# Kernel tuning notes

Hardware: AMD Instinct MI355X
Metric: run time of the kernel (lower is better)

The kernel has to match this reference:

```python
import jax, jax.numpy as jnp
import numpy as np

N = 50000      # nodes
E = 800000     # edges (avg degree 16)
H = 128        # hidden_dim
ED = 8         # edge_dim
TD = 64        # time_dim
EIN = 2 * H + 1 + ED + TD  # 329, phi_e input dim


def _linear_params(key, fan_in, fan_out):
    kw, kb = jax.random.split(key)
    s = 1.0 / np.sqrt(fan_in)
    W = jax.random.uniform(kw, (fan_in, fan_out), minval=-s, maxval=s, dtype=jnp.float32)
    b = jax.random.uniform(kb, (fan_out,), minval=-s, maxval=s, dtype=jnp.float32)
    return W, b


def setup_inputs() -> dict:
    key = jax.random.key(0)
    ks = jax.random.split(key, 12)
    h = jax.random.normal(ks[0], (N, H), dtype=jnp.float32)
    x = jax.random.normal(ks[1], (N, 3), dtype=jnp.float32)
    edge_attr = jax.random.normal(ks[2], (E, ED), dtype=jnp.float32)
    t_emb = jax.random.normal(ks[3], (N, TD), dtype=jnp.float32)
    edge_index = jax.random.randint(ks[4], (2, E), 0, N, dtype=jnp.int32)
    We1_w, We1_b = _linear_params(ks[5], EIN, H)
    We2_w, We2_b = _linear_params(ks[6], H, H)
    Watt_w, Watt_b = _linear_params(ks[7], H, 1)
    Wx1_w, Wx1_b = _linear_params(ks[8], H, H)
    Wx2_w, Wx2_b = _linear_params(ks[9], H, 1)
    Wh1_w, Wh1_b = _linear_params(ks[10], 2 * H, H)
    Wh2_w, Wh2_b = _linear_params(ks[11], H, H)
    return dict(h=h, x=x, edge_attr=edge_attr, t_emb=t_emb,
                We1_w=We1_w, We1_b=We1_b, We2_w=We2_w, We2_b=We2_b,
                Watt_w=Watt_w, Watt_b=Watt_b,
                Wx1_w=Wx1_w, Wx1_b=Wx1_b, Wx2_w=Wx2_w, Wx2_b=Wx2_b,
                Wh1_w=Wh1_w, Wh1_b=Wh1_b, Wh2_w=Wh2_w, Wh2_b=Wh2_b,
                edge_index=edge_index)


def reference(h, x, edge_attr, t_emb,
              We1_w, We1_b, We2_w, We2_b,
              Watt_w, Watt_b,
              Wx1_w, Wx1_b, Wx2_w, Wx2_b,
              Wh1_w, Wh1_b, Wh2_w, Wh2_b,
              edge_index):
    src, dst = edge_index[0], edge_index[1]
    diff = x[src] - x[dst]                                   # (E, 3)
    dist_sq = jnp.sum(diff * diff, axis=-1, keepdims=True)   # (E, 1)
    # m_ij = phi_e(h_i || h_j || ||x_i - x_j||^2 || edge_attr || t_emb)
    msg_in = jnp.concatenate([h[src], h[dst], dist_sq, edge_attr, t_emb[src]], axis=-1)  # (E, EIN)
    m = jax.nn.silu(msg_in @ We1_w + We1_b) @ We2_w + We2_b  # (E, H)
    # attention gate
    att = jax.nn.sigmoid(m @ Watt_w + Watt_b)                # (E, 1)
    m = att * m
    # equivariant coordinate update
    coord_w = jnp.tanh(jax.nn.silu(m @ Wx1_w + Wx1_b) @ Wx2_w + Wx2_b)  # (E, 1)
    coord_shift = diff * coord_w                             # (E, 3)
    coord_agg = jax.ops.segment_sum(coord_shift, dst, num_segments=N)   # (N, 3)
    deg = jax.ops.segment_sum(jnp.ones((dst.shape[0], 1), dtype=x.dtype), dst, num_segments=N)
    x_out = x + coord_agg / (deg + 1.0)
    # invariant feature update with residual
    msg_agg = jax.ops.segment_sum(m, dst, num_segments=N)    # (N, H)
    h_in = jnp.concatenate([h, msg_agg], axis=-1)            # (N, 2H)
    h_out = h + (jax.nn.silu(h_in @ Wh1_w + Wh1_b) @ Wh2_w + Wh2_b)
    return (h_out, x_out)
```

## Files before the change

### kernel.cpp

```cpp
#include <hip/hip_runtime.h>
#include <hip/hip_fp16.h>

typedef unsigned short u16;
typedef unsigned int u32;
typedef __attribute__((ext_vector_type(8))) short short8;
typedef __attribute__((ext_vector_type(4))) float f32x4;

#define NN 50000
#define EE 800000

__device__ __forceinline__ float bf2f(u16 u){ union{u32 i; float f;} v; v.i=((u32)u)<<16; return v.f; }
__device__ __forceinline__ u16 f2bf(float f){ union{float f; u32 i;} v; v.f=f; u32 b=v.i; b += 0x7FFFu + ((b>>16)&1u); return (u16)(b>>16); }
__device__ __forceinline__ float sigmoidf_(float x){ return 1.0f/(1.0f+__expf(-x)); }

__device__ __forceinline__ void cvt8(uint4 q, float* f){
  f[0]=bf2f((u16)(q.x&0xFFFF)); f[1]=bf2f((u16)(q.x>>16));
  f[2]=bf2f((u16)(q.y&0xFFFF)); f[3]=bf2f((u16)(q.y>>16));
  f[4]=bf2f((u16)(q.z&0xFFFF)); f[5]=bf2f((u16)(q.z>>16));
  f[6]=bf2f((u16)(q.w&0xFFFF)); f[7]=bf2f((u16)(q.w>>16));
}
__device__ __forceinline__ uint4 pack8(const float* f){
  uint4 q;
  q.x=(u32)f2bf(f[0])|((u32)f2bf(f[1])<<16);
  q.y=(u32)f2bf(f[2])|((u32)f2bf(f[3])<<16);
  q.z=(u32)f2bf(f[4])|((u32)f2bf(f[5])<<16);
  q.w=(u32)f2bf(f[6])|((u32)f2bf(f[7])<<16);
  return q;
}

__device__ __forceinline__ float h2f(u16 u){ __half h; *reinterpret_cast<u16*>(&h)=u; return (float)h; }
__device__ __forceinline__ u32 f2h2pack(float lo, float hi){
  __half2 h2 = __floats2half2_rn(lo, hi);
  return *reinterpret_cast<u32*>(&h2);
}
__device__ __forceinline__ void atomic_pk_add_f16(u16* addr, u32 data){
  asm volatile("global_atomic_pk_add_f16 %0, %1, off" :: "v"(addr), "v"(data) : "memory");
}

template<int FP32> struct IO;
template<> struct IO<0> {
  static __device__ __forceinline__ float ld(const void* p, int i){ return bf2f(((const u16*)p)[i]); }
  static __device__ __forceinline__ void ld8(const void* p, int i, float* f){
    cvt8(*(const uint4*)((const u16*)p + i), f);
  }
  static __device__ __forceinline__ void st(void* p, int i, float v){ ((u16*)p)[i] = f2bf(v); }
};
template<> struct IO<1> {
  static __device__ __forceinline__ float ld(const void* p, int i){ return ((const float*)p)[i]; }
  static __device__ __forceinline__ void ld8(const void* p, int i, float* f){
    f32x4 a = *(const f32x4*)((const float*)p + i);
    f32x4 b = *(const f32x4*)((const float*)p + i + 4);
    f[0]=a[0]; f[1]=a[1]; f[2]=a[2]; f[3]=a[3];
    f[4]=b[0]; f[5]=b[1]; f[6]=b[2]; f[7]=b[3];
  }
  static __device__ __forceinline__ void st(void* p, int i, float v){ ((float*)p)[i] = v; }
};

__device__ __forceinline__ void atomic_add_bf16pair(u32* addr, float lo, float hi){
  u32 old = *addr, assumed;
  do {
    assumed = old;
    float flo = bf2f((u16)(assumed & 0xFFFFu)) + lo;
    float fhi = bf2f((u16)(assumed >> 16)) + hi;
    u32 newv = (u32)f2bf(flo) | ((u32)f2bf(fhi) << 16);
    if (newv == assumed) return;
    old = atomicCAS(addr, assumed, newv);
  } while (old != assumed);
}

__global__ void k_probe(const u16* __restrict__ hraw, int* __restrict__ flag){
  if (threadIdx.x==0 && blockIdx.x==0){
    float mx = 0.f; int zc = 0;
    for (int i = 0; i < 256; i += 2){
      u16 u = hraw[i];
      if (u == 0) zc++;
      float v = fabsf(bf2f(u));
      mx = fmaxf(mx, v);
    }
    flag[0] = (mx > 1e3f || zc > 32) ? 1 : 0;
  }
}

template<int FP32>
__global__ __launch_bounds__(256) void k_prep(
    const int* __restrict__ flag,
    const void* __restrict__ We1, const void* __restrict__ We2,
    const void* __restrict__ Wx1, const void* __restrict__ Wh1,
    const void* __restrict__ Wh2,
    u16* __restrict__ WprojT, u16* __restrict__ We2T, u16* __restrict__ Wx1T,
    u16* __restrict__ Wh1T, u16* __restrict__ Wh2T, u16* __restrict__ Wrk9T)
{
  if (flag[0] != FP32) return;
  int i = blockIdx.x*256 + threadIdx.x;
  if (i < 49152){
    int n = i/192, k = i%192; float v;
    if (n < 128) v = (k<128) ? IO<FP32>::ld(We1, k*128+n) : IO<FP32>::ld(We1, (265+k-128)*128+n);
    else         v = (k<128) ? IO<FP32>::ld(We1, (128+k)*128+(n-128)) : 0.f;
    WprojT[i] = f2bf(v);
  } else if (i < 65536){
    int j=i-49152; int n=j/128, k=j%128; We2T[j] = f2bf(IO<FP32>::ld(We2, k*128+n));
  } else if (i < 81920){
    int j=i-65536; int n=j/128, k=j%128; Wx1T[j] = f2bf(IO<FP32>::ld(Wx1, k*128+n));
  } else if (i < 114688){
    int j=i-81920; int n=j/256, k=j%256; Wh1T[j] = f2bf(IO<FP32>::ld(Wh1, k*128+n));
  } else if (i < 131072){
    int j=i-114688; int n=j/128, k=j%128; Wh2T[j] = f2bf(IO<FP32>::ld(Wh2, k*128+n));
  } else if (i < 135168){
    int j=i-131072; int n=j/32, k=j%32;
    float v = (k<=8) ? IO<FP32>::ld(We1, (256+k)*128+n) : 0.f;
    Wrk9T[j] = f2bf(v);
  }
}

template<int FP32, int WP2>
__global__ __launch_bounds__(256) void k_proj(
    const int* __restrict__ flag,
    const void* __restrict__ h, const void* __restrict__ temb,
    const u16* __restrict__ WprojT, const void* __restrict__ We1b,
    u16* __restrict__ P13, u16* __restrict__ P2)
{
  if (flag[0] != FP32) return;
  constexpr int NT = WP2 ? 16 : 8;
  __shared__ __align__(16) u16 s_a[64][200];
  int tid = threadIdx.x; int nbase = blockIdx.x*64;
  {
    u32* p = (u32*)&s_a[0][0];
    for (int i = tid; i < 6400; i += 256) p[i] = 0u;
  }
  __syncthreads();
  {
    int r = tid>>2, p = tid&3; int node = nbase + r;
    if (node < NN){
      #pragma unroll
      for (int c=0;c<6;c++){
        int col = p*48 + c*8;
        float f[8];
        if (col<128) IO<FP32>::ld8(h, node*128 + col, f);
        else         IO<FP32>::ld8(temb, node*64 + (col-128), f);
        *(uint4*)&s_a[r][col] = pack8(f);
      }
    }
  }
  __syncthreads();
  int lane=tid&63, wid=tid>>6, quad=lane>>4, l15=lane&15, mb=wid*16;
  f32x4 acc[NT];
  #pragma unroll
  for (int nt=0;nt<NT;nt++) acc[nt]=(f32x4){0.f,0.f,0.f,0.f};
  #pragma unroll
  for (int ks=0;ks<6;ks++){
    short8 af = *(const short8*)&s_a[mb+l15][ks*32+quad*8];
    #pragma unroll
    for (int nt=0;nt<NT;nt++){
      short8 bfr = *(const short8*)(WprojT + (nt*16+l15)*192 + ks*32+quad*8);
      acc[nt] = __builtin_amdgcn_mfma_f32_16x16x32_bf16(af, bfr, acc[nt], 0,0,0);
    }
  }
  #pragma unroll
  for (int r=0;r<4;r++){
    int node = nbase + mb + quad*4 + r;
    if (node < NN){
      #pragma unroll
      for (int nt=0;nt<NT;nt++){
        int colg = nt*16 + l15;
        float v = acc[nt][r];
        if (colg < 128) P13[node*128+colg] = f2bf(v + IO<FP32>::ld(We1b, colg));
        else if (WP2)   P2[node*128+(colg-128)] = f2bf(v);
      }
    }
  }
}

template<int FP32, int TIERA>
__global__ __launch_bounds__(256, 6) void k_edge(
    const int* __restrict__ flag,
    const void* __restrict__ x, const void* __restrict__ ea,
    const void* __restrict__ We1, const void* __restrict__ h,
    const void* __restrict__ We2b, const void* __restrict__ Watt, const void* __restrict__ Wattb,
    const void* __restrict__ Wx1b, const void* __restrict__ Wx2, const void* __restrict__ Wx2b,
    const int* __restrict__ eidx,
    const u16* __restrict__ P13, const u16* __restrict__ P2,
    const u16* __restrict__ WprojT, const u16* __restrict__ Wrk9T,
    const u16* __restrict__ We2T, const u16* __restrict__ Wx1T,
    u16* __restrict__ msgh, u16* __restrict__ msgb, float* __restrict__ cagg)
{
  if (flag[0] != FP32) return;
  __shared__ int s_dst[64];
  __shared__ float s_dif[64][3];
  __shared__ __align__(16) u16 s_hid[64][136];
  __shared__ __align__(16) u16 s_att[TIERA?64:1][40];
  __shared__ __align__(16) u16 s_m[TIERA?1:64][136];
  __shared__ __align__(16) u16 s_hd[TIERA?1:64][136];
  int tid = threadIdx.x;
  int ebase = blockIdx.x*64;
  {
    int el = tid>>2, p = tid&3;
    int srcI = eidx[ebase+el], dstI = eidx[EE+ebase+el];
    float d0 = IO<FP32>::ld(x, srcI*3+0) - IO<FP32>::ld(x, dstI*3+0);
    float d1 = IO<FP32>::ld(x, srcI*3+1) - IO<FP32>::ld(x, dstI*3+1);
    float d2 = IO<FP32>::ld(x, srcI*3+2) - IO<FP32>::ld(x, dstI*3+2);
    float dsq = d0*d0 + d1*d1 + d2*d2;
    if (p==0){ s_dst[el]=dstI; s_dif[el][0]=d0; s_dif[el][1]=d1; s_dif[el][2]=d2; }
    if constexpr (TIERA){
      if (p < 2){
        float eav[8]; IO<FP32>::ld8(ea, (ebase+el)*8, eav);
        float f9[8];
        if (p==0){ f9[0]=dsq; for (int t=0;t<7;t++) f9[1+t]=eav[t]; }
        else { f9[0]=eav[7]; for (int t=1;t<8;t++) f9[t]=0.f; }
        *(uint4*)&s_att[el][p*8] = pack8(f9);
      } else {
        *(uint4*)&s_att[el][p*8] = make_uint4(0,0,0,0);
      }
      const u16* p13r = P13 + srcI*128;
      const u16* p2r  = P2  + dstI*128;
      #pragma unroll
      for (int c=0;c<4;c++){
        int col = p*32 + c*8;
        float fa[8], fb[8];
        cvt8(*(const uint4*)(p13r+col), fa);
        cvt8(*(const uint4*)(p2r+col),  fb);
        #pragma unroll
        for (int i2=0;i2<8;i2++) fa[i2] += fb[i2];
        *(uint4*)&s_hid[el][col] = pack8(fa);
      }
    } else {
      float eav[8]; IO<FP32>::ld8(ea, (ebase+el)*8, eav);
      const u16* p13r = P13 + srcI*128;
      #pragma unroll
      for (int c=0;c<4;c++){
        int col = p*32 + c*8;
        float fw[8], pre[8];
        cvt8(*(const uint4*)(p13r+col), pre);
        IO<FP32>::ld8(We1, 256*128 + col, fw);
        #pragma unroll
        for (int i2=0;i2<8;i2++) pre[i2] += dsq*fw[i2];
        #pragma unroll
        for (int t=0;t<8;t++){
          IO<FP32>::ld8(We1, (257+t)*128 + col, fw);
          #pragma unroll
          for (int i2=0;i2<8;i2++) pre[i2] += eav[t]*fw[i2];
        }
        *(uint4*)&s_hid[el][col] = pack8(pre);
        float hd[8]; IO<FP32>::ld8(h, dstI*128 + col, hd);
        *(uint4*)&s_hd[el][col] = pack8(hd);
      }
    }
  }
  int lane=tid&63, wid=tid>>6, quad=lane>>4, l15=lane&15, mb=wid*16;
  if constexpr (TIERA){
    f32x4 acc9[8];
    #pragma unroll
    for (int nt=0;nt<8;nt++) acc9[nt]=(f32x4){0.f,0.f,0.f,0.f};
    short8 a9 = *(const short8*)&s_att[mb+l15][quad*8];
    #pragma unroll
    for (int nt=0;nt<8;nt++){
      short8 bfr = *(const short8*)(Wrk9T + (nt*16+l15)*32 + quad*8);
      acc9[nt] = __builtin_amdgcn_mfma_f32_16x16x32_bf16(a9, bfr, acc9[nt], 0,0,0);
    }
    #pragma unroll
    for (int r=0;r<4;r++){
      int row = mb + quad*4 + r;
      #pragma unroll
      for (int nt=0;nt<8;nt++){
        int col = nt*16+l15;
        float u = bf2f(s_hid[row][col]) + acc9[nt][r];
        u = u*sigmoidf_(u);
        s_hid[row][col] = f2bf(u);
      }
    }
  } else {
    f32x4 accg[8];
    #pragma unroll
    for (int nt=0;nt<8;nt++) accg[nt]=(f32x4){0.f,0.f,0.f,0.f};
    #pragma unroll
    for (int ks=0;ks<4;ks++){
      short8 af = *(const short8*)&s_hd[mb+l15][ks*32+quad*8];
      #pragma unroll
      for (int nt=0;nt<8;nt++){
        short8 bfr = *(const short8*)(WprojT + (128 + nt*16+l15)*192 + ks*32+quad*8);
        accg[nt] = __builtin_amdgcn_mfma_f32_16x16x32_bf16(af, bfr, accg[nt], 0,0,0);
      }
    }
    #pragma unroll
    for (int r=0;r<4;r++){
      int row = mb + quad*4 + r;
      #pragma unroll
      for (int nt=0;nt<8;nt++){
        int col = nt*16+l15;
        float u = bf2f(s_hid[row][col]) + accg[nt][r];
        u = u*sigmoidf_(u);
        s_hid[row][col] = f2bf(u);
      }
    }
  }
  f32x4 acc[8];
  #pragma unroll
  for (int nt=0;nt<8;nt++) acc[nt]=(f32x4){0.f,0.f,0.f,0.f};
  #pragma unroll
  for (int ks=0;ks<4;ks++){
    short8 af = *(const short8*)&s_hid[mb+l15][ks*32+quad*8];
    #pragma unroll
    for (int nt=0;nt<8;nt++){
      short8 bfr = *(const short8*)(We2T + (nt*16+l15)*128 + ks*32+quad*8);
      acc[nt] = __builtin_amdgcn_mfma_f32_16x16x32_bf16(af, bfr, acc[nt], 0,0,0);
    }
  }
  float b2v[8], wav[8];
  #pragma unroll
  for (int nt=0;nt<8;nt++){ b2v[nt]=IO<FP32>::ld(We2b, nt*16+l15); wav[nt]=IO<FP32>::ld(Watt, nt*16+l15); }
  float attb = IO<FP32>::ld(Wattb, 0);
  float mval[8][4]; float dotr[4];
  #pragma unroll
  for (int r=0;r<4;r++){
    float s=0.f;
    #pragma unroll
    for (int nt=0;nt<8;nt++){ mval[nt][r]=acc[nt][r]+b2v[nt]; s += mval[nt][r]*wav[nt]; }
    dotr[r]=s;
  }
  #pragma unroll
  for (int off=1;off<16;off<<=1){
    #pragma unroll
    for (int r=0;r<4;r++) dotr[r] += __shfl_xor(dotr[r], off);
  }
  #pragma unroll
  for (int r=0;r<4;r++){
    float att = sigmoidf_(dotr[r]+attb);
    int erow = mb + quad*4 + r;
    int dstN = s_dst[erow];
    #pragma unroll
    for (int nt=0;nt<8;nt++){
      float v = mval[nt][r]*att;
      mval[nt][r] = v;
      if constexpr (TIERA){
        s_hid[erow][nt*16+l15] = f2bf(v);
      } else {
        s_m[erow][nt*16+l15] = f2bf(v);
      }
    }
    if constexpr (TIERA){
      #pragma unroll
      for (int nt=0;nt<8;nt++){
        float part = __shfl_xor(mval[nt][r], 1);
        if ((l15 & 1) == 0){
          atomic_pk_add_f16(msgh + dstN*128 + nt*16 + l15, f2h2pack(mval[nt][r], part));
        }
      }
    } else {
      #pragma unroll
      for (int nt=0;nt<8;nt++){
        float part = __shfl_xor(mval[nt][r], 1);
        if ((l15 & 1) == 0){
          atomic_add_bf16pair((u32*)(msgb + dstN*128 + nt*16 + l15), mval[nt][r], part);
        }
      }
    }
  }
  f32x4 acc2[8];
  #pragma unroll
  for (int nt=0;nt<8;nt++) acc2[nt]=(f32x4){0.f,0.f,0.f,0.f};
  #pragma unroll
  for (int ks=0;ks<4;ks++){
    short8 af = TIERA ? *(const short8*)&s_hid[mb+l15][ks*32+quad*8]
                      : *(const short8*)&s_m[mb+l15][ks*32+quad*8];
    #pragma unroll
    for (int nt=0;nt<8;nt++){
      short8 bfr = *(const short8*)(Wx1T + (nt*16+l15)*128 + ks*32+quad*8);
      acc2[nt] = __builtin_amdgcn_mfma_f32_16x16x32_bf16(af, bfr, acc2[nt], 0,0,0);
    }
  }
  float bx1v[8], wx2v[8];
  #pragma unroll
  for (int nt=0;nt<8;nt++){ bx1v[nt]=IO<FP32>::ld(Wx1b, nt*16+l15); wx2v[nt]=IO<FP32>::ld(Wx2, nt*16+l15); }
  float bx2f = IO<FP32>::ld(Wx2b, 0);
  float dc[4];
  #pragma unroll
  for (int r=0;r<4;r++){
    float s=0.f;
    #pragma unroll
    for (int nt=0;nt<8;nt++){
      float u = acc2[nt][r] + bx1v[nt];
      u = u*sigmoidf_(u);
      s += u*wx2v[nt];
    }
    dc[r]=s;
  }
  #pragma unroll
  for (int off=1;off<16;off<<=1){
    #pragma unroll
    for (int r=0;r<4;r++) dc[r] += __shfl_xor(dc[r], off);
  }
  #pragma unroll
  for (int r=0;r<4;r++){
    float cw = tanhf(dc[r]+bx2f);
    if (l15==0){
      int erow = mb + quad*4 + r;
      int dstN = s_dst[erow];
      atomicAdd(&cagg[dstN*4+0], s_dif[erow][0]*cw);
      atomicAdd(&cagg[dstN*4+1], s_dif[erow][1]*cw);
      atomicAdd(&cagg[dstN*4+2], s_dif[erow][2]*cw);
      atomicAdd(&cagg[dstN*4+3], 1.0f);
    }
  }
}

template<int FP32, int MSGF>
__global__ __launch_bounds__(256) void k_node(
    const int* __restrict__ flag,
    const void* __restrict__ h, const void* __restrict__ x,
    const u16* __restrict__ msgh, const u16* __restrict__ msgb,
    const float* __restrict__ cagg,
    const u16* __restrict__ Wh1T, const void* __restrict__ Wh1b,
    const u16* __restrict__ Wh2T, const void* __restrict__ Wh2b,
    void* __restrict__ out)
{
  if (flag[0] != FP32) return;
  __shared__ __align__(16) u16 s_a[64][264];
  __shared__ __align__(16) u16 s_u[64][136];
  int tid = threadIdx.x; int nbase = blockIdx.x*64;
  {
    u32* p1 = (u32*)&s_a[0][0];
    for (int i = tid; i < 8448; i += 256) p1[i] = 0u;
  }
  __syncthreads();
  {
    int r = tid>>2, p = tid&3; int node = nbase + r;
    if (node < NN){
      #pragma unroll
      for (int c=0;c<8;c++){
        int col = p*64 + c*8;
        if (col < 128){
          float f[8]; IO<FP32>::ld8(h, node*128 + col, f);
          *(uint4*)&s_a[r][col] = pack8(f);
        } else if (MSGF){
          uint4 q = *(const uint4*)(msgh + node*128 + (col-128));
          float f[8];
          f[0]=h2f((u16)(q.x&0xFFFF)); f[1]=h2f((u16)(q.x>>16));
          f[2]=h2f((u16)(q.y&0xFFFF)); f[3]=h2f((u16)(q.y>>16));
          f[4]=h2f((u16)(q.z&0xFFFF)); f[5]=h2f((u16)(q.z>>16));
          f[6]=h2f((u16)(q.w&0xFFFF)); f[7]=h2f((u16)(q.w>>16));
          *(uint4*)&s_a[r][col] = pack8(f);
        } else {
          *(uint4*)&s_a[r][col] = *(const uint4*)(msgb + node*128 + (col-128));
        }
      }
    }
  }
  __syncthreads();
  int lane=tid&63, wid=tid>>6, quad=lane>>4, l15=lane&15, mb=wid*16;
  f32x4 acc[8];
  #pragma unroll
  for (int nt=0;nt<8;nt++) acc[nt]=(f32x4){0.f,0.f,0.f,0.f};
  #pragma unroll
  for (int ks=0;ks<8;ks++){
    short8 af = *(const short8*)&s_a[mb+l15][ks*32+quad*8];
    #pragma unroll
    for (int nt=0;nt<8;nt++){
      short8 bfr = *(const short8*)(Wh1T + (nt*16+l15)*256 + ks*32+quad*8);
      acc[nt] = __builtin_amdgcn_mfma_f32_16x16x32_bf16(af, bfr, acc[nt], 0,0,0);
    }
  }
  #pragma unroll
  for (int r=0;r<4;r++){
    int row = mb + quad*4 + r;
    #pragma unroll
    for (int nt=0;nt<8;nt++){
      int col = nt*16+l15;
      float u = acc[nt][r] + IO<FP32>::ld(Wh1b, col);
      u = u*sigmoidf_(u);
      s_u[row][col] = f2bf(u);
    }
  }
  f32x4 acc2[8];
  #pragma unroll
  for (int nt=0;nt<8;nt++) acc2[nt]=(f32x4){0.f,0.f,0.f,0.f};
  #pragma unroll
  for (int ks=0;ks<4;ks++){
    short8 af = *(const short8*)&s_u[mb+l15][ks*32+quad*8];
    #pragma unroll
    for (int nt=0;nt<8;nt++){
      short8 bfr = *(const short8*)(Wh2T + (nt*16+l15)*128 + ks*32+quad*8);
      acc2[nt] = __builtin_amdgcn_mfma_f32_16x16x32_bf16(af, bfr, acc2[nt], 0,0,0);
    }
  }
  #pragma unroll
  for (int r=0;r<4;r++){
    int node = nbase + mb + quad*4 + r;
    if (node < NN){
      #pragma unroll
      for (int nt=0;nt<8;nt++){
        int col = nt*16+l15;
        float v = IO<FP32>::ld(h, node*128+col) + acc2[nt][r] + IO<FP32>::ld(Wh2b, col);
        IO<FP32>::st(out, node*128+col, v);
      }
    }
  }
  if (tid < 64){
    int node = nbase + tid;
    if (node < NN){
      float inv = 1.0f/(cagg[node*4+3] + 1.0f);
      #pragma unroll
      for (int c=0;c<3;c++){
        float v = IO<FP32>::ld(x, node*3+c) + cagg[node*4+c]*inv;
        IO<FP32>::st(out, NN*128 + node*3 + c, v);
      }
    }
  }
}

extern "C" void kernel_launch(void* const* d_in, const int* in_sizes, int n_in,
                              void* d_out, int out_size, void* d_ws, size_t ws_size,
                              hipStream_t stream) {
  const void* h     = d_in[0];
  const void* x     = d_in[1];
  const void* ea    = d_in[2];
  const void* temb  = d_in[3];
  const void* We1   = d_in[4];
  const void* We1b  = d_in[5];
  const void* We2   = d_in[6];
  const void* We2b  = d_in[7];
  const void* Watt  = d_in[8];
  const void* Wattb = d_in[9];
  const void* Wx1   = d_in[10];
  const void* Wx1b  = d_in[11];
  const void* Wx2   = d_in[12];
  const void* Wx2b  = d_in[13];
  const void* Wh1   = d_in[14];
  const void* Wh1b  = d_in[15];
  const void* Wh2   = d_in[16];
  const void* Wh2b  = d_in[17];
  const int* eidx   = (const int*)d_in[18];
  char* ws = (char*)d_ws;

  u16* WprojT = (u16*)(ws + 0);
  u16* We2T   = (u16*)(ws + 98304);
  u16* Wx1T   = (u16*)(ws + 131072);
  u16* Wh1T   = (u16*)(ws + 163840);
  u16* Wh2T   = (u16*)(ws + 229376);
  u16* Wrk9T  = (u16*)(ws + 262144);
  float* cagg = (float*)(ws + 270336);
  int* flag   = (int*)(ws + 1070336);
  bool tierA = (ws_size >= (size_t)39470592);
  u16* msgh   = (u16*)(ws + 1070592);
  u16* msgb   = (u16*)(ws + 1070592);
  u16* P2     = (u16*)(ws + 26670592);
  u16* P13    = (u16*)d_out;

  hipMemsetAsync(ws + 270336, 0, 13600256, stream);
  k_probe<<<1, 64, 0, stream>>>((const u16*)h, flag);
  k_prep<0><<<528, 256, 0, stream>>>(flag, We1, We2, Wx1, Wh1, Wh2, WprojT, We2T, Wx1T, Wh1T, Wh2T, Wrk9T);
  k_prep<1><<<528, 256, 0, stream>>>(flag, We1, We2, Wx1, Wh1, Wh2, WprojT, We2T, Wx1T, Wh1T, Wh2T, Wrk9T);
  if (tierA){
    k_proj<0,1><<<(NN+63)/64, 256, 0, stream>>>(flag, h, temb, WprojT, We1b, P13, P2);
    k_proj<1,1><<<(NN+63)/64, 256, 0, stream>>>(flag, h, temb, WprojT, We1b, P13, P2);
    k_edge<0,1><<<EE/64, 256, 0, stream>>>(flag, x, ea, We1, h, We2b, Watt, Wattb, Wx1b, Wx2, Wx2b,
                                           eidx, P13, P2, WprojT, Wrk9T, We2T, Wx1T, msgh, msgb, cagg);
    k_edge<1,1><<<EE/64, 256, 0, stream>>>(flag, x, ea, We1, h, We2b, Watt, Wattb, Wx1b, Wx2, Wx2b,
                                           eidx, P13, P2, WprojT, Wrk9T, We2T, Wx1T, msgh, msgb, cagg);
    k_node<0,1><<<(NN+63)/64, 256, 0, stream>>>(flag, h, x, msgh, msgb, cagg, Wh1T, Wh1b, Wh2T, Wh2b, d_out);
    k_node<1,1><<<(NN+63)/64, 256, 0, stream>>>(flag, h, x, msgh, msgb, cagg, Wh1T, Wh1b, Wh2T, Wh2b, d_out);
  } else {
    k_proj<0,0><<<(NN+63)/64, 256, 0, stream>>>(flag, h, temb, WprojT, We1b, P13, P2);
    k_proj<1,0><<<(NN+63)/64, 256, 0, stream>>>(flag, h, temb, WprojT, We1b, P13, P2);
    k_edge<0,0><<<EE/64, 256, 0, stream>>>(flag, x, ea, We1, h, We2b, Watt, Wattb, Wx1b, Wx2, Wx2b,
                                           eidx, P13, P2, WprojT, Wrk9T, We2T, Wx1T, msgh, msgb, cagg);
    k_edge<1,0><<<EE/64, 256, 0, stream>>>(flag, x, ea, We1, h, We2b, Watt, Wattb, Wx1b, Wx2, Wx2b,
                                           eidx, P13, P2, WprojT, Wrk9T, We2T, Wx1T, msgh, msgb, cagg);
    k_node<0,0><<<(NN+63)/64, 256, 0, stream>>>(flag, h, x, msgh, msgb, cagg, Wh1T, Wh1b, Wh2T, Wh2b, d_out);
    k_node<1,0><<<(NN+63)/64, 256, 0, stream>>>(flag, h, x, msgh, msgb, cagg, Wh1T, Wh1b, Wh2T, Wh2b, d_out);
  }
}
```

Measured before the change: 888.4 us.

## Sort edges by destination and combine per-destination atomics in edge kernel

Adds a counting sort of edges by destination: histogram, three-stage scan and atomic scatter into a permutation array. The edge kernel then walks edges in destination order and accumulates consecutive rows that share a destination in registers, so it issues fewer global atomic adds for messages and coordinates. Node degree now comes from the row offsets instead of an atomic counter. The cost is several extra preprocessing launches, more workspace, and an indirect load through the permutation for edge attributes.

```diff
diff --git a/kernel.cpp b/kernel.cpp
--- a/kernel.cpp
+++ b/kernel.cpp
@@ -8,6 +8,7 @@
 
 #define NN 50000
 #define EE 800000
+#define SCAN_B 49
 
 __device__ __forceinline__ float bf2f(u16 u){ union{u32 i; float f;} v; v.i=((u32)u)<<16; return v.f; }
 __device__ __forceinline__ u16 f2bf(float f){ union{float f; u32 i;} v; v.f=f; u32 b=v.i; b += 0x7FFFu + ((b>>16)&1u); return (u16)(b>>16); }
@@ -78,6 +79,49 @@
       mx = fmaxf(mx, v);
     }
     flag[0] = (mx > 1e3f || zc > 32) ? 1 : 0;
+  }
+}
+
+__global__ __launch_bounds__(256) void k_hist(const int* __restrict__ eidx, int* __restrict__ cnt){
+  int e = blockIdx.x*256 + threadIdx.x;
+  if (e < EE) atomicAdd(&cnt[eidx[EE+e]], 1);
+}
+__global__ __launch_bounds__(1024) void k_scanA(const int* __restrict__ cnt,
+                                               int* __restrict__ rowoff, int* __restrict__ bsum){
+  __shared__ int s[1024];
+  int t = threadIdx.x, b = blockIdx.x, i = b*1024 + t;
+  int v = (i < NN) ? cnt[i] : 0;
+  s[t] = v; __syncthreads();
+  #pragma unroll
+  for (int off=1; off<1024; off<<=1){
+    int add = (t>=off) ? s[t-off] : 0;
+    __syncthreads();
+    s[t] += add;
+    __syncthreads();
+  }
+  rowoff[i+1] = s[t];
+  if (t==1023) bsum[b] = s[t];
+}
+__global__ void k_scanB(int* __restrict__ bsum){
+  if (threadIdx.x==0 && blockIdx.x==0){
+    int acc=0;
+    for (int b=0;b<SCAN_B;b++){ int v=bsum[b]; bsum[b]=acc; acc+=v; }
+  }
+}
+__global__ __launch_bounds__(1024) void k_scanC(int* __restrict__ rowoff, int* __restrict__ cur,
+                                               const int* __restrict__ bsum){
+  int t = threadIdx.x, b = blockIdx.x, i = b*1024 + t;
+  int v = rowoff[i+1] + bsum[b];
+  rowoff[i+1] = v;
+  if (i < NN-1) cur[i+1] = v;
+  if (i==0){ rowoff[0]=0; cur[0]=0; }
+}
+__global__ __launch_bounds__(256) void k_scatter(const int* __restrict__ eidx,
+                                                 int* __restrict__ cur, int* __restrict__ perm){
+  int e = blockIdx.x*256 + threadIdx.x;
+  if (e < EE){
+    int p = atomicAdd(&cur[eidx[EE+e]], 1);
+    perm[p] = e;
   }
 }
 
@@ -177,7 +221,7 @@
     const void* __restrict__ We1, const void* __restrict__ h,
     const void* __restrict__ We2b, const void* __restrict__ Watt, const void* __restrict__ Wattb,
     const void* __restrict__ Wx1b, const void* __restrict__ Wx2, const void* __restrict__ Wx2b,
-    const int* __restrict__ eidx,
+    const int* __restrict__ eidx, const int* __restrict__ perm,
     const u16* __restrict__ P13, const u16* __restrict__ P2,
     const u16* __restrict__ WprojT, const u16* __restrict__ Wrk9T,
     const u16* __restrict__ We2T, const u16* __restrict__ Wx1T,
@@ -194,7 +238,8 @@
   int ebase = blockIdx.x*64;
   {
     int el = tid>>2, p = tid&3;
-    int srcI = eidx[ebase+el], dstI = eidx[EE+ebase+el];
+    int e = TIERA ? perm[ebase+el] : (ebase+el);
+    int srcI = eidx[e], dstI = eidx[EE+e];
     float d0 = IO<FP32>::ld(x, srcI*3+0) - IO<FP32>::ld(x, dstI*3+0);
     float d1 = IO<FP32>::ld(x, srcI*3+1) - IO<FP32>::ld(x, dstI*3+1);
     float d2 = IO<FP32>::ld(x, srcI*3+2) - IO<FP32>::ld(x, dstI*3+2);
@@ -202,7 +247,7 @@
     if (p==0){ s_dst[el]=dstI; s_dif[el][0]=d0; s_dif[el][1]=d1; s_dif[el][2]=d2; }
     if constexpr (TIERA){
       if (p < 2){
-        float eav[8]; IO<FP32>::ld8(ea, (ebase+el)*8, eav);
+        float eav[8]; IO<FP32>::ld8(ea, e*8, eav);
         float f9[8];
         if (p==0){ f9[0]=dsq; for (int t=0;t<7;t++) f9[1+t]=eav[t]; }
         else { f9[0]=eav[7]; for (int t=1;t<8;t++) f9[t]=0.f; }
@@ -223,7 +268,7 @@
         *(uint4*)&s_hid[el][col] = pack8(fa);
       }
     } else {
-      float eav[8]; IO<FP32>::ld8(ea, (ebase+el)*8, eav);
+      float eav[8]; IO<FP32>::ld8(ea, e*8, eav);
       const u16* p13r = P13 + srcI*128;
       #pragma unroll
       for (int c=0;c<4;c++){
@@ -321,30 +366,46 @@
     #pragma unroll
     for (int r=0;r<4;r++) dotr[r] += __shfl_xor(dotr[r], off);
   }
-  #pragma unroll
-  for (int r=0;r<4;r++){
-    float att = sigmoidf_(dotr[r]+attb);
-    int erow = mb + quad*4 + r;
-    int dstN = s_dst[erow];
-    #pragma unroll
-    for (int nt=0;nt<8;nt++){
-      float v = mval[nt][r]*att;
-      mval[nt][r] = v;
-      if constexpr (TIERA){
+  if constexpr (TIERA){
+    float racc[8];
+    #pragma unroll
+    for (int nt=0;nt<8;nt++) racc[nt]=0.f;
+    #pragma unroll
+    for (int r=0;r<4;r++){
+      float att = sigmoidf_(dotr[r]+attb);
+      int erow = mb + quad*4 + r;
+      int dstN = s_dst[erow];
+      bool emit = (r==3) || (s_dst[erow+1] != dstN);
+      #pragma unroll
+      for (int nt=0;nt<8;nt++){
+        float v = mval[nt][r]*att;
         s_hid[erow][nt*16+l15] = f2bf(v);
-      } else {
+        racc[nt] += v;
+      }
+      #pragma unroll
+      for (int nt=0;nt<8;nt++){
+        float part = __shfl_xor(racc[nt], 1);
+        if (emit && ((l15 & 1) == 0)){
+          atomic_pk_add_f16(msgh + dstN*128 + nt*16 + l15, f2h2pack(racc[nt], part));
+        }
+      }
+      if (emit){
+        #pragma unroll
+        for (int nt=0;nt<8;nt++) racc[nt]=0.f;
+      }
+    }
+  } else {
+    #pragma unroll
+    for (int r=0;r<4;r++){
+      float att = sigmoidf_(dotr[r]+attb);
+      int erow = mb + quad*4 + r;
+      int dstN = s_dst[erow];
+      #pragma unroll
+      for (int nt=0;nt<8;nt++){
+        float v = mval[nt][r]*att;
+        mval[nt][r] = v;
         s_m[erow][nt*16+l15] = f2bf(v);
       }
-    }
-    if constexpr (TIERA){
-      #pragma unroll
-      for (int nt=0;nt<8;nt++){
-        float part = __shfl_xor(mval[nt][r], 1);
-        if ((l15 & 1) == 0){
-          atomic_pk_add_f16(msgh + dstN*128 + nt*16 + l15, f2h2pack(mval[nt][r], part));
-        }
-      }
-    } else {
       #pragma unroll
       for (int nt=0;nt<8;nt++){
         float part = __shfl_xor(mval[nt][r], 1);
@@ -388,16 +449,38 @@
     #pragma unroll
     for (int r=0;r<4;r++) dc[r] += __shfl_xor(dc[r], off);
   }
-  #pragma unroll
-  for (int r=0;r<4;r++){
-    float cw = tanhf(dc[r]+bx2f);
+  if constexpr (TIERA){
     if (l15==0){
-      int erow = mb + quad*4 + r;
-      int dstN = s_dst[erow];
-      atomicAdd(&cagg[dstN*4+0], s_dif[erow][0]*cw);
-      atomicAdd(&cagg[dstN*4+1], s_dif[erow][1]*cw);
-      atomicAdd(&cagg[dstN*4+2], s_dif[erow][2]*cw);
-      atomicAdd(&cagg[dstN*4+3], 1.0f);
+      float c0=0.f, c1=0.f, c2=0.f;
+      #pragma unroll
+      for (int r=0;r<4;r++){
+        float cw = tanhf(dc[r]+bx2f);
+        int erow = mb + quad*4 + r;
+        int dstN = s_dst[erow];
+        c0 += s_dif[erow][0]*cw;
+        c1 += s_dif[erow][1]*cw;
+        c2 += s_dif[erow][2]*cw;
+        bool emit = (r==3) || (s_dst[erow+1] != dstN);
+        if (emit){
+          atomicAdd(&cagg[dstN*4+0], c0);
+          atomicAdd(&cagg[dstN*4+1], c1);
+          atomicAdd(&cagg[dstN*4+2], c2);
+          c0=c1=c2=0.f;
+        }
+      }
+    }
+  } else {
+    #pragma unroll
+    for (int r=0;r<4;r++){
+      float cw = tanhf(dc[r]+bx2f);
+      if (l15==0){
+        int erow = mb + quad*4 + r;
+        int dstN = s_dst[erow];
+        atomicAdd(&cagg[dstN*4+0], s_dif[erow][0]*cw);
+        atomicAdd(&cagg[dstN*4+1], s_dif[erow][1]*cw);
+        atomicAdd(&cagg[dstN*4+2], s_dif[erow][2]*cw);
+        atomicAdd(&cagg[dstN*4+3], 1.0f);
+      }
     }
   }
 }
@@ -407,7 +490,7 @@
     const int* __restrict__ flag,
     const void* __restrict__ h, const void* __restrict__ x,
     const u16* __restrict__ msgh, const u16* __restrict__ msgb,
-    const float* __restrict__ cagg,
+    const float* __restrict__ cagg, const int* __restrict__ rowoff,
     const u16* __restrict__ Wh1T, const void* __restrict__ Wh1b,
     const u16* __restrict__ Wh2T, const void* __restrict__ Wh2b,
     void* __restrict__ out)
@@ -496,7 +579,8 @@
   if (tid < 64){
     int node = nbase + tid;
     if (node < NN){
-      float inv = 1.0f/(cagg[node*4+3] + 1.0f);
+      float deg = MSGF ? (float)(rowoff[node+1]-rowoff[node]) : cagg[node*4+3];
+      float inv = 1.0f/(deg + 1.0f);
       #pragma unroll
       for (int c=0;c<3;c++){
         float v = IO<FP32>::ld(x, node*3+c) + cagg[node*4+c]*inv;
@@ -541,30 +625,43 @@
   bool tierA = (ws_size >= (size_t)39470592);
   u16* msgh   = (u16*)(ws + 1070592);
   u16* msgb   = (u16*)(ws + 1070592);
-  u16* P2     = (u16*)(ws + 26670592);
+  u16* P2     = (u16*)(ws + 13870592);
+  int* cnt    = (int*)(ws + 26670592);
+  int* rowoff = (int*)(ws + 26871296);
+  int* cur    = (int*)(ws + 27072512);
+  int* bsum   = (int*)(ws + 27273216);
+  int* perm   = (int*)(ws + 27273472);
   u16* P13    = (u16*)d_out;
 
   hipMemsetAsync(ws + 270336, 0, 13600256, stream);
   k_probe<<<1, 64, 0, stream>>>((const u16*)h, flag);
+  if (tierA){
+    hipMemsetAsync(cnt, 0, 200704, stream);
+    k_hist<<<(EE+255)/256, 256, 0, stream>>>(eidx, cnt);
+    k_scanA<<<SCAN_B, 1024, 0, stream>>>(cnt, rowoff, bsum);
+    k_scanB<<<1, 64, 0, stream>>>(bsum);
+    k_scanC<<<SCAN_B, 1024, 0, stream>>>(rowoff, cur, bsum);
+    k_scatter<<<(EE+255)/256, 256, 0, stream>>>(eidx, cur, perm);
+  }
   k_prep<0><<<528, 256, 0, stream>>>(flag, We1, We2, Wx1, Wh1, Wh2, WprojT, We2T, Wx1T, Wh1T, Wh2T, Wrk9T);
   k_prep<1><<<528, 256, 0, stream>>>(flag, We1, We2, Wx1, Wh1, Wh2, WprojT, We2T, Wx1T, Wh1T, Wh2T, Wrk9T);
   if (tierA){
     k_proj<0,1><<<(NN+63)/64, 256, 0, stream>>>(flag, h, temb, WprojT, We1b, P13, P2);
     k_proj<1,1><<<(NN+63)/64, 256, 0, stream>>>(flag, h, temb, WprojT, We1b, P13, P2);
     k_edge<0,1><<<EE/64, 256, 0, stream>>>(flag, x, ea, We1, h, We2b, Watt, Wattb, Wx1b, Wx2, Wx2b,
-                                           eidx, P13, P2, WprojT, Wrk9T, We2T, Wx1T, msgh, msgb, cagg);
+                                           eidx, perm, P13, P2, WprojT, Wrk9T, We2T, Wx1T, msgh, msgb, cagg);
     k_edge<1,1><<<EE/64, 256, 0, stream>>>(flag, x, ea, We1, h, We2b, Watt, Wattb, Wx1b, Wx2, Wx2b,
-                                           eidx, P13, P2, WprojT, Wrk9T, We2T, Wx1T, msgh, msgb, cagg);
-    k_node<0,1><<<(NN+63)/64, 256, 0, stream>>>(flag, h, x, msgh, msgb, cagg, Wh1T, Wh1b, Wh2T, Wh2b, d_out);
-    k_node<1,1><<<(NN+63)/64, 256, 0, stream>>>(flag, h, x, msgh, msgb, cagg, Wh1T, Wh1b, Wh2T, Wh2b, d_out);
+                                           eidx, perm, P13, P2, WprojT, Wrk9T, We2T, Wx1T, msgh, msgb, cagg);
+    k_node<0,1><<<(NN+63)/64, 256, 0, stream>>>(flag, h, x, msgh, msgb, cagg, rowoff, Wh1T, Wh1b, Wh2T, Wh2b, d_out);
+    k_node<1,1><<<(NN+63)/64, 256, 0, stream>>>(flag, h, x, msgh, msgb, cagg, rowoff, Wh1T, Wh1b, Wh2T, Wh2b, d_out);
   } else {
     k_proj<0,0><<<(NN+63)/64, 256, 0, stream>>>(flag, h, temb, WprojT, We1b, P13, P2);
     k_proj<1,0><<<(NN+63)/64, 256, 0, stream>>>(flag, h, temb, WprojT, We1b, P13, P2);
     k_edge<0,0><<<EE/64, 256, 0, stream>>>(flag, x, ea, We1, h, We2b, Watt, Wattb, Wx1b, Wx2, Wx2b,
-                                           eidx, P13, P2, WprojT, Wrk9T, We2T, Wx1T, msgh, msgb, cagg);
+                                           eidx, perm, P13, P2, WprojT, Wrk9T, We2T, Wx1T, msgh, msgb, cagg);
     k_edge<1,0><<<EE/64, 256, 0, stream>>>(flag, x, ea, We1, h, We2b, Watt, Wattb, Wx1b, Wx2, Wx2b,
-                                           eidx, P13, P2, WprojT, Wrk9T, We2T, Wx1T, msgh, msgb, cagg);
-    k_node<0,0><<<(NN+63)/64, 256, 0, stream>>>(flag, h, x, msgh, msgb, cagg, Wh1T, Wh1b, Wh2T, Wh2b, d_out);
-    k_node<1,0><<<(NN+63)/64, 256, 0, stream>>>(flag, h, x, msgh, msgb, cagg, Wh1T, Wh1b, Wh2T, Wh2b, d_out);
-  }
-}
+                                           eidx, perm, P13, P2, WprojT, Wrk9T, We2T, Wx1T, msgh, msgb, cagg);
+    k_node<0,0><<<(NN+63)/64, 256, 0, stream>>>(flag, h, x, msgh, msgb, cagg, rowoff, Wh1T, Wh1b, Wh2T, Wh2b, d_out);
+    k_node<1,0><<<(NN+63)/64, 256, 0, stream>>>(flag, h, x, msgh, msgb, cagg, rowoff, Wh1T, Wh1b, Wh2T, Wh2b, d_out);
+  }
+}
```

New measurement: 945.9 us. 1.06x slower.
